# Kernel tuning notes

Hardware: AMD Instinct MI355X
Metric: run time of the kernel (lower is better)

Reference implementation:

```python
import jax, jax.numpy as jnp
import numpy as np

B, S, D, H = 2, 2048, 1024, 16
HD = D // H  # 64


def setup_inputs() -> dict:
    key = jax.random.key(0)
    ks = jax.random.split(key, 10)
    sc = 1.0 / np.sqrt(D)
    return {
        "decoder_hs": jax.random.normal(ks[0], (B, S, D), jnp.float32),
        "encoder_hs": jax.random.normal(ks[1], (B, S, D), jnp.float32),
        "Wq": jax.random.normal(ks[2], (D, D), jnp.float32) * sc,
        "bq": jax.random.normal(ks[3], (D,), jnp.float32) * 0.02,
        "Wk": jax.random.normal(ks[4], (D, D), jnp.float32) * sc,
        "bk": jax.random.normal(ks[5], (D,), jnp.float32) * 0.02,
        "Wv": jax.random.normal(ks[6], (D, D), jnp.float32) * sc,
        "bv": jax.random.normal(ks[7], (D,), jnp.float32) * 0.02,
        "Wp": jax.random.normal(ks[8], (D, D), jnp.float32) * sc,
        "bp": jax.random.normal(ks[9], (D,), jnp.float32) * 0.02,
    }


def reference(decoder_hs, encoder_hs, Wq, bq, Wk, bk, Wv, bv, Wp, bp):
    b, s, d = decoder_hs.shape
    # torch nn.Linear: y = x @ W.T + b, W is [out, in]
    q = decoder_hs @ Wq.T + bq
    k = encoder_hs @ Wk.T + bk
    v = encoder_hs @ Wv.T + bv
    # head split: [b, s, d] -> [b, h, s, hd]
    q = q.reshape(b, s, H, HD).transpose(0, 2, 1, 3)
    k = k.reshape(b, s, H, HD).transpose(0, 2, 1, 3)
    v = v.reshape(b, s, H, HD).transpose(0, 2, 1, 3)
    scale = 1.0 / np.sqrt(HD).astype(np.float32)
    att = jnp.einsum('bhqd,bhkd->bhqk', q, k) * scale
    att = jax.nn.softmax(att, axis=-1)
    y = jnp.einsum('bhqk,bhkd->bhqd', att, v)
    y = y.transpose(0, 2, 1, 3).reshape(b, s, d)
    return y @ Wp.T + bp
```

## Files before the change

kernel.cpp:

```cpp
#include <hip/hip_runtime.h>
#include <hip/hip_bf16.h>
#include <cstdint>
#include <cstddef>

#define BB 2
#define SS 2048
#define DD 1024
#define HH 16
#define HD 64

typedef __attribute__((ext_vector_type(8))) short bf16x8;
typedef __attribute__((ext_vector_type(4))) short bf16x4;
typedef __attribute__((ext_vector_type(4))) float f32x4;

#define MFMA16(va, vb, c) __builtin_amdgcn_mfma_f32_16x16x16bf16_1k(va, vb, c, 0, 0, 0)

#define GLL(g, l) __builtin_amdgcn_global_load_lds( \
    (const __attribute__((address_space(1))) void*)(g), \
    (__attribute__((address_space(3))) void*)(l), 16, 0, 0)

__device__ __forceinline__ short f2bf_fast(float f) {
    uint32_t u = __float_as_uint(f);
    u += 0x7FFF + ((u >> 16) & 1);
    return (short)(u >> 16);
}
__device__ __forceinline__ uint32_t pack_bf2(float a, float b) {
    uint32_t ua = __float_as_uint(a), ub = __float_as_uint(b);
    ua += 0x7FFF + ((ua >> 16) & 1);
    ub += 0x7FFF + ((ub >> 16) & 1);
    return (ua >> 16) | (ub & 0xFFFF0000u);
}
__device__ __forceinline__ bf16x8 cvt8(const float* __restrict__ p) {
    float4 a = *(const float4*)p;
    float4 b = *(const float4*)(p + 4);
    union { uint32_t d[4]; bf16x8 v; } r;
    r.d[0] = pack_bf2(a.x, a.y);
    r.d[1] = pack_bf2(a.z, a.w);
    r.d[2] = pack_bf2(b.x, b.y);
    r.d[3] = pack_bf2(b.z, b.w);
    return r.v;
}

__global__ __launch_bounds__(256) void cvt6_kernel(
    const float* __restrict__ s0, const float* __restrict__ s1,
    const float* __restrict__ s2, const float* __restrict__ s3,
    const float* __restrict__ s4, const float* __restrict__ s5,
    short* __restrict__ d0, short* __restrict__ d1, short* __restrict__ d2,
    short* __restrict__ d3, short* __restrict__ d4, short* __restrict__ d5)
{
    const int z = blockIdx.z;
    const float* s = (z == 0) ? s0 : (z == 1) ? s1 : (z == 2) ? s2
                   : (z == 3) ? s3 : (z == 4) ? s4 : s5;
    short* d = (z == 0) ? d0 : (z == 1) ? d1 : (z == 2) ? d2
             : (z == 3) ? d3 : (z == 4) ? d4 : d5;
    const int n8 = (z < 2) ? (BB * SS * DD / 8) : (DD * DD / 8);
    const int id = blockIdx.x * 256 + threadIdx.x;
    if (id >= n8) return;
    bf16x8 r = cvt8(s + (size_t)id * 8);
    *(uint4*)(d + (size_t)id * 8) = *(uint4*)&r;
}

template<int BF>
__global__ __launch_bounds__(256, 3) void qkv_gemm_kernel(
    const void* __restrict__ dec, const void* __restrict__ enc,
    const void* __restrict__ Wq, const void* __restrict__ Wk,
    const void* __restrict__ Wv,
    const float* __restrict__ bq, const float* __restrict__ bk,
    const float* __restrict__ bv,
    short* __restrict__ Qo, short* __restrict__ Ko, short* __restrict__ Vo)
{
    __shared__ short As[128 * 32];
    __shared__ short Bs[128 * 32];

    const int z = blockIdx.z;
    const void* Xv = (z == 0) ? dec : enc;
    const void* Wp_ = (z == 0) ? Wq : (z == 1) ? Wk : Wv;
    const float* bias = (z == 0) ? bq : (z == 1) ? bk : bv;
    short* Yo = (z == 0) ? Qo : (z == 1) ? Ko : Vo;

    const int t = threadIdx.x;
    const int lane = t & 63, wv = t >> 6;
    const int lr = lane & 15, quad = lane >> 4;
    const int wm = wv >> 1, wn = wv & 1;
    const int m0 = blockIdx.y * 128;
    const int n0 = blockIdx.x * 128;
    const int K = DD;

    f32x4 acc[4][4];
    #pragma unroll
    for (int i = 0; i < 4; i++)
        #pragma unroll
        for (int j = 0; j < 4; j++) acc[i][j] = (f32x4){0.f, 0.f, 0.f, 0.f};

    for (int kb = 0; kb < K; kb += 32) {
        __syncthreads();
        if (BF) {
            const short* Xb = (const short*)Xv;
            const short* Wb = (const short*)Wp_;
            #pragma unroll
            for (int c = 0; c < 2; c++) {
                int r0 = wv * 32 + c * 16;
                int r = r0 + (lane >> 2), ch = (lane & 3) * 8;
                GLL(Xb + (size_t)(m0 + r) * K + kb + ch, &As[r0 * 32]);
                GLL(Wb + (size_t)(n0 + r) * K + kb + ch, &Bs[r0 * 32]);
            }
        } else {
            const float* Xf = (const float*)Xv;
            const float* Wf = (const float*)Wp_;
            #pragma unroll
            for (int c = 0; c < 2; c++) {
                int id = t + c * 256;
                int r = id >> 2, c8 = (id & 3) * 8;
                *(bf16x8*)&As[r * 32 + c8] = cvt8(Xf + (size_t)(m0 + r) * K + kb + c8);
                *(bf16x8*)&Bs[r * 32 + c8] = cvt8(Wf + (size_t)(n0 + r) * K + kb + c8);
            }
        }
        __syncthreads();

        bf16x8 af[4], bfr[4];
        #pragma unroll
        for (int mi = 0; mi < 4; mi++)
            af[mi] = *(const bf16x8*)&As[(wm * 64 + mi * 16 + lr) * 32 + quad * 8];
        #pragma unroll
        for (int ni = 0; ni < 4; ni++)
            bfr[ni] = *(const bf16x8*)&Bs[(wn * 64 + ni * 16 + lr) * 32 + quad * 8];
        #pragma unroll
        for (int mi = 0; mi < 4; mi++)
            #pragma unroll
            for (int ni = 0; ni < 4; ni++)
                acc[mi][ni] = __builtin_amdgcn_mfma_f32_16x16x32_bf16(
                    af[mi], bfr[ni], acc[mi][ni], 0, 0, 0);
    }

    if (z < 2) {
        #pragma unroll
        for (int ni = 0; ni < 4; ni++) {
            int col = n0 + wn * 64 + ni * 16 + lr;
            int h = col >> 6, hd = col & 63;
            float bvv = bias[col];
            #pragma unroll
            for (int mi = 0; mi < 4; mi++) {
                #pragma unroll
                for (int r2 = 0; r2 < 4; r2++) {
                    int row = m0 + wm * 64 + mi * 16 + quad * 4 + r2;
                    int b = row >> 11, s = row & 2047;
                    float v = acc[mi][ni][r2] + bvv;
                    size_t off = ((size_t)(b * HH + h) * SS + s) * HD + hd;
                    Yo[off] = f2bf_fast(v);
                }
            }
        }
    } else {
        #pragma unroll
        for (int ni = 0; ni < 4; ni++) {
            int col = n0 + wn * 64 + ni * 16 + lr;
            int h = col >> 6, hd = col & 63;
            float bvv = bias[col];
            #pragma unroll
            for (int mi = 0; mi < 4; mi++) {
                int s0 = m0 + wm * 64 + mi * 16 + quad * 4;
                int b = s0 >> 11, s = s0 & 2047;
                union { uint32_t d[2]; } u;
                u.d[0] = pack_bf2(acc[mi][ni][0] + bvv, acc[mi][ni][1] + bvv);
                u.d[1] = pack_bf2(acc[mi][ni][2] + bvv, acc[mi][ni][3] + bvv);
                size_t off = ((size_t)(b * HH + h) * HD + hd) * SS + s;
                *(uint2*)(Yo + off) = *(uint2*)&u;
            }
        }
    }
}

template<int WBF>
__global__ __launch_bounds__(256, 2) void proj_gemm_kernel(
    const short* __restrict__ X,
    const void* __restrict__ W, const float* __restrict__ bias,
    float* __restrict__ Y)
{
    __shared__ short As[64 * 32];
    __shared__ short Bs[128 * 32];

    const int t = threadIdx.x;
    const int lane = t & 63, wv = t >> 6;
    const int lr = lane & 15, quad = lane >> 4;
    const int wm = wv >> 1, wn = wv & 1;
    const int m0 = blockIdx.y * 64;
    const int n0 = blockIdx.x * 128;
    const int K = DD, N = DD;

    f32x4 acc[2][4];
    #pragma unroll
    for (int i = 0; i < 2; i++)
        #pragma unroll
        for (int j = 0; j < 4; j++) acc[i][j] = (f32x4){0.f, 0.f, 0.f, 0.f};

    for (int kb = 0; kb < K; kb += 32) {
        __syncthreads();
        {
            int r0 = wv * 16;
            int r = r0 + (lane >> 2), ch = (lane & 3) * 8;
            GLL(X + (size_t)(m0 + r) * K + kb + ch, &As[r0 * 32]);
        }
        if (WBF) {
            const short* Wb = (const short*)W;
            #pragma unroll
            for (int c = 0; c < 2; c++) {
                int r0 = wv * 32 + c * 16;
                int r = r0 + (lane >> 2), ch = (lane & 3) * 8;
                GLL(Wb + (size_t)(n0 + r) * K + kb + ch, &Bs[r0 * 32]);
            }
        } else {
            const float* Wf = (const float*)W;
            #pragma unroll
            for (int c = 0; c < 2; c++) {
                int id = t + c * 256;
                int r = id >> 2, c8 = (id & 3) * 8;
                *(bf16x8*)&Bs[r * 32 + c8] = cvt8(Wf + (size_t)(n0 + r) * K + kb + c8);
            }
        }
        __syncthreads();

        bf16x8 af[2], bfr[4];
        #pragma unroll
        for (int mi = 0; mi < 2; mi++)
            af[mi] = *(const bf16x8*)&As[(wm * 32 + mi * 16 + lr) * 32 + quad * 8];
        #pragma unroll
        for (int ni = 0; ni < 4; ni++)
            bfr[ni] = *(const bf16x8*)&Bs[(wn * 64 + ni * 16 + lr) * 32 + quad * 8];
        #pragma unroll
        for (int mi = 0; mi < 2; mi++)
            #pragma unroll
            for (int ni = 0; ni < 4; ni++)
                acc[mi][ni] = __builtin_amdgcn_mfma_f32_16x16x32_bf16(
                    af[mi], bfr[ni], acc[mi][ni], 0, 0, 0);
    }

    #pragma unroll
    for (int ni = 0; ni < 4; ni++) {
        int col = n0 + wn * 64 + ni * 16 + lr;
        float bvv = bias[col];
        #pragma unroll
        for (int mi = 0; mi < 2; mi++) {
            #pragma unroll
            for (int r2 = 0; r2 < 4; r2++) {
                int row = m0 + wm * 32 + mi * 16 + quad * 4 + r2;
                Y[(size_t)row * N + col] = acc[mi][ni][r2] + bvv;
            }
        }
    }
}

__global__ __launch_bounds__(256, 2) void attn_kernel(
    const short* __restrict__ Q,
    const short* __restrict__ Kgl,
    const short* __restrict__ Vt_g,
    short* __restrict__ Y)
{
    __shared__ short Ks[128][72];
    __shared__ short Vt[64][136];

    const int t = threadIdx.x;
    const int lane = t & 63, w = t >> 6;
    const int lr = lane & 15, quad = lane >> 4;

    const int qt = blockIdx.x & 15;
    const int bh = blockIdx.x >> 4;
    const int b = bh >> 4, h = bh & 15;

    const float C = 0.125f * 1.44269504088896f;

    const short* QpA = Q + ((size_t)bh * SS + qt * 128 + w * 32 + lr) * HD;
    const short* QpB = QpA + 16 * HD;
    bf16x8 qfA0 = *(const bf16x8*)(QpA + quad * 8);
    bf16x8 qfA1 = *(const bf16x8*)(QpA + 32 + quad * 8);
    bf16x8 qfB0 = *(const bf16x8*)(QpB + quad * 8);
    bf16x8 qfB1 = *(const bf16x8*)(QpB + 32 + quad * 8);

    f32x4 oA[4], oB[4];
    #pragma unroll
    for (int i = 0; i < 4; i++) {
        oA[i] = (f32x4){0.f, 0.f, 0.f, 0.f};
        oB[i] = (f32x4){0.f, 0.f, 0.f, 0.f};
    }
    float lsumA = 0.f, lsumB = 0.f;

    const uint4* Kg0 = (const uint4*)(Kgl + (size_t)bh * SS * HD);
    const short* Vg0 = Vt_g + (size_t)bh * HD * SS;

    for (int kt = 0; kt < SS / 128; kt++) {
        __syncthreads();
        const uint4* Kg = Kg0 + (size_t)kt * 128 * 8;
        #pragma unroll
        for (int c = 0; c < 4; c++) {
            int id = t + c * 256;
            int row = id >> 3, h8 = id & 7;
            *(uint4*)&Ks[row][h8 * 8] = Kg[id];
        }
        #pragma unroll
        for (int c = 0; c < 4; c++) {
            int id = t + c * 256;
            int hd = id >> 4, s16 = id & 15;
            *(uint4*)&Vt[hd][s16 * 8] =
                *(const uint4*)(Vg0 + (size_t)hd * SS + kt * 128 + s16 * 8);
        }
        __syncthreads();

        f32x4 scA[8], scB[8];
        #pragma unroll
        for (int nt = 0; nt < 8; nt++) {
            bf16x8 kf0 = *(const bf16x8*)&Ks[nt * 16 + lr][quad * 8];
            bf16x8 kf1 = *(const bf16x8*)&Ks[nt * 16 + lr][32 + quad * 8];
            scA[nt] = __builtin_amdgcn_mfma_f32_16x16x32_bf16(
                kf0, qfA0, (f32x4){0.f, 0.f, 0.f, 0.f}, 0, 0, 0);
            scA[nt] = __builtin_amdgcn_mfma_f32_16x16x32_bf16(kf1, qfA1, scA[nt], 0, 0, 0);
            scB[nt] = __builtin_amdgcn_mfma_f32_16x16x32_bf16(
                kf0, qfB0, (f32x4){0.f, 0.f, 0.f, 0.f}, 0, 0, 0);
            scB[nt] = __builtin_amdgcn_mfma_f32_16x16x32_bf16(kf1, qfB1, scB[nt], 0, 0, 0);
        }

        bf16x4 pbA[8], pbB[8];
        #pragma unroll
        for (int nt = 0; nt < 8; nt++) {
            float a0 = __builtin_amdgcn_exp2f(scA[nt][0] * C);
            float a1 = __builtin_amdgcn_exp2f(scA[nt][1] * C);
            float a2 = __builtin_amdgcn_exp2f(scA[nt][2] * C);
            float a3 = __builtin_amdgcn_exp2f(scA[nt][3] * C);
            lsumA += (a0 + a1) + (a2 + a3);
            union { uint32_t d[2]; bf16x4 v; } ua;
            ua.d[0] = pack_bf2(a0, a1);
            ua.d[1] = pack_bf2(a2, a3);
            pbA[nt] = ua.v;
            float b0 = __builtin_amdgcn_exp2f(scB[nt][0] * C);
            float b1 = __builtin_amdgcn_exp2f(scB[nt][1] * C);
            float b2 = __builtin_amdgcn_exp2f(scB[nt][2] * C);
            float b3 = __builtin_amdgcn_exp2f(scB[nt][3] * C);
            lsumB += (b0 + b1) + (b2 + b3);
            union { uint32_t d[2]; bf16x4 v; } ub;
            ub.d[0] = pack_bf2(b0, b1);
            ub.d[1] = pack_bf2(b2, b3);
            pbB[nt] = ub.v;
        }

        #pragma unroll
        for (int dt = 0; dt < 4; dt++) {
            #pragma unroll
            for (int nt = 0; nt < 8; nt++) {
                bf16x4 va = *(const bf16x4*)&Vt[dt * 16 + lr][nt * 16 + quad * 4];
                oA[dt] = MFMA16(va, pbA[nt], oA[dt]);
                oB[dt] = MFMA16(va, pbB[nt], oB[dt]);
            }
        }
    }

    lsumA += __shfl_xor(lsumA, 16, 64);
    lsumA += __shfl_xor(lsumA, 32, 64);
    lsumB += __shfl_xor(lsumB, 16, 64);
    lsumB += __shfl_xor(lsumB, 32, 64);
    float invA = 1.0f / lsumA, invB = 1.0f / lsumB;

    const int srowA = qt * 128 + w * 32 + lr;
    short* YpA = Y + ((size_t)b * SS + srowA) * DD + h * 64 + quad * 4;
    short* YpB = YpA + 16 * DD;
    #pragma unroll
    for (int dt = 0; dt < 4; dt++) {
        union { uint32_t d[2]; } ua;
        ua.d[0] = pack_bf2(oA[dt][0] * invA, oA[dt][1] * invA);
        ua.d[1] = pack_bf2(oA[dt][2] * invA, oA[dt][3] * invA);
        *(uint2*)(YpA + dt * 16) = *(uint2*)&ua;
        union { uint32_t d[2]; } ub;
        ub.d[0] = pack_bf2(oB[dt][0] * invB, oB[dt][1] * invB);
        ub.d[1] = pack_bf2(oB[dt][2] * invB, oB[dt][3] * invB);
        *(uint2*)(YpB + dt * 16) = *(uint2*)&ub;
    }
}

extern "C" void kernel_launch(void* const* d_in, const int* in_sizes, int n_in,
                              void* d_out, int out_size, void* d_ws, size_t ws_size,
                              hipStream_t stream) {
    const float* dec = (const float*)d_in[0];
    const float* enc = (const float*)d_in[1];
    const float* Wq  = (const float*)d_in[2];
    const float* bq  = (const float*)d_in[3];
    const float* Wk  = (const float*)d_in[4];
    const float* bk  = (const float*)d_in[5];
    const float* Wv  = (const float*)d_in[6];
    const float* bv  = (const float*)d_in[7];
    const float* Wp  = (const float*)d_in[8];
    const float* bp  = (const float*)d_in[9];

    const size_t per = (size_t)BB * HH * SS * HD;
    const size_t wsz = (size_t)DD * DD;
    short* ws = (short*)d_ws;
    short* Qb  = ws;
    short* Kb  = ws + per;
    short* Vtb = ws + 2 * per;
    short* Yb  = ws + 3 * per;

    dim3 qkv_grid(DD / 128, (BB * SS) / 128, 3);
    dim3 proj_grid(DD / 128, (BB * SS) / 64);
    const int attn_blocks = BB * HH * (SS / 128);

    const size_t need = (6 * per + 4 * wsz) * sizeof(short);
    if (ws_size >= need) {
        short* decb = ws + 4 * per;
        short* encb = ws + 5 * per;
        short* Wqb  = ws + 6 * per;
        short* Wkb  = Wqb + wsz;
        short* Wvb  = Wqb + 2 * wsz;
        short* Wpb  = Wqb + 3 * wsz;
        cvt6_kernel<<<dim3((BB * SS * DD / 8 + 255) / 256, 1, 6), 256, 0, stream>>>(
            dec, enc, Wq, Wk, Wv, Wp, decb, encb, Wqb, Wkb, Wvb, Wpb);
        qkv_gemm_kernel<1><<<qkv_grid, 256, 0, stream>>>(
            decb, encb, Wqb, Wkb, Wvb, bq, bk, bv, Qb, Kb, Vtb);
        attn_kernel<<<attn_blocks, 256, 0, stream>>>(Qb, Kb, Vtb, Yb);
        proj_gemm_kernel<1><<<proj_grid, 256, 0, stream>>>(Yb, Wpb, bp, (float*)d_out);
    } else {
        qkv_gemm_kernel<0><<<qkv_grid, 256, 0, stream>>>(
            dec, enc, Wq, Wk, Wv, bq, bk, bv, Qb, Kb, Vtb);
        attn_kernel<<<attn_blocks, 256, 0, stream>>>(Qb, Kb, Vtb, Yb);
        proj_gemm_kernel<0><<<proj_grid, 256, 0, stream>>>(Yb, Wp, bp, (float*)d_out);
    }
}
```

Measured before the change: 215.3 us.

## Prefetch K/V tiles into registers and add mid-workspace bf16 weight path

The attention kernel now loads the next K and V tiles into registers while computing on the current tile, so global load latency overlaps with the MFMA work. The workspace layout is reduced: bf16 activation copies now reuse the Y slot, which lowers the full-path requirement. A new intermediate path converts only the weights to bf16 when the workspace cannot hold activation copies, with the GEMM templated separately on activation and weight precision. The prefetch costs extra registers per thread and may reduce occupancy in the attention kernel.

```diff
diff --git a/kernel.cpp b/kernel.cpp
--- a/kernel.cpp
+++ b/kernel.cpp
@@ -60,7 +60,21 @@
     *(uint4*)(d + (size_t)id * 8) = *(uint4*)&r;
 }
 
-template<int BF>
+__global__ __launch_bounds__(256) void cvtW_kernel(
+    const float* __restrict__ s0, const float* __restrict__ s1,
+    const float* __restrict__ s2, const float* __restrict__ s3,
+    short* __restrict__ d0, short* __restrict__ d1,
+    short* __restrict__ d2, short* __restrict__ d3)
+{
+    const int z = blockIdx.z;
+    const float* s = (z == 0) ? s0 : (z == 1) ? s1 : (z == 2) ? s2 : s3;
+    short* d = (z == 0) ? d0 : (z == 1) ? d1 : (z == 2) ? d2 : d3;
+    const int id = blockIdx.x * 256 + threadIdx.x;
+    bf16x8 r = cvt8(s + (size_t)id * 8);
+    *(uint4*)(d + (size_t)id * 8) = *(uint4*)&r;
+}
+
+template<int XBF, int WBF>
 __global__ __launch_bounds__(256, 3) void qkv_gemm_kernel(
     const void* __restrict__ dec, const void* __restrict__ enc,
     const void* __restrict__ Wq, const void* __restrict__ Wk,
@@ -94,24 +108,37 @@
 
     for (int kb = 0; kb < K; kb += 32) {
         __syncthreads();
-        if (BF) {
+        if (XBF) {
             const short* Xb = (const short*)Xv;
-            const short* Wb = (const short*)Wp_;
             #pragma unroll
             for (int c = 0; c < 2; c++) {
                 int r0 = wv * 32 + c * 16;
                 int r = r0 + (lane >> 2), ch = (lane & 3) * 8;
                 GLL(Xb + (size_t)(m0 + r) * K + kb + ch, &As[r0 * 32]);
-                GLL(Wb + (size_t)(n0 + r) * K + kb + ch, &Bs[r0 * 32]);
             }
         } else {
             const float* Xf = (const float*)Xv;
-            const float* Wf = (const float*)Wp_;
             #pragma unroll
             for (int c = 0; c < 2; c++) {
                 int id = t + c * 256;
                 int r = id >> 2, c8 = (id & 3) * 8;
                 *(bf16x8*)&As[r * 32 + c8] = cvt8(Xf + (size_t)(m0 + r) * K + kb + c8);
+            }
+        }
+        if (WBF) {
+            const short* Wb = (const short*)Wp_;
+            #pragma unroll
+            for (int c = 0; c < 2; c++) {
+                int r0 = wv * 32 + c * 16;
+                int r = r0 + (lane >> 2), ch = (lane & 3) * 8;
+                GLL(Wb + (size_t)(n0 + r) * K + kb + ch, &Bs[r0 * 32]);
+            }
+        } else {
+            const float* Wf = (const float*)Wp_;
+            #pragma unroll
+            for (int c = 0; c < 2; c++) {
+                int id = t + c * 256;
+                int r = id >> 2, c8 = (id & 3) * 8;
                 *(bf16x8*)&Bs[r * 32 + c8] = cvt8(Wf + (size_t)(n0 + r) * K + kb + c8);
             }
         }
@@ -286,21 +313,42 @@
     const uint4* Kg0 = (const uint4*)(Kgl + (size_t)bh * SS * HD);
     const short* Vg0 = Vt_g + (size_t)bh * HD * SS;
 
-    for (int kt = 0; kt < SS / 128; kt++) {
-        __syncthreads();
-        const uint4* Kg = Kg0 + (size_t)kt * 128 * 8;
-        #pragma unroll
-        for (int c = 0; c < 4; c++) {
-            int id = t + c * 256;
-            int row = id >> 3, h8 = id & 7;
-            *(uint4*)&Ks[row][h8 * 8] = Kg[id];
-        }
+    uint4 kreg[4], vreg[4];
+    {
+        const uint4* Kg = Kg0;
+        #pragma unroll
+        for (int c = 0; c < 4; c++) kreg[c] = Kg[t + c * 256];
         #pragma unroll
         for (int c = 0; c < 4; c++) {
             int id = t + c * 256;
             int hd = id >> 4, s16 = id & 15;
-            *(uint4*)&Vt[hd][s16 * 8] =
-                *(const uint4*)(Vg0 + (size_t)hd * SS + kt * 128 + s16 * 8);
+            vreg[c] = *(const uint4*)(Vg0 + (size_t)hd * SS + s16 * 8);
+        }
+    }
+
+    for (int kt = 0; kt < SS / 128; kt++) {
+        __syncthreads();
+        #pragma unroll
+        for (int c = 0; c < 4; c++) {
+            int id = t + c * 256;
+            *(uint4*)&Ks[id >> 3][(id & 7) * 8] = kreg[c];
+        }
+        #pragma unroll
+        for (int c = 0; c < 4; c++) {
+            int id = t + c * 256;
+            int hd = id >> 4, s16 = id & 15;
+            *(uint4*)&Vt[hd][s16 * 8] = vreg[c];
+        }
+        if (kt + 1 < SS / 128) {
+            const uint4* Kg = Kg0 + (size_t)(kt + 1) * 1024;
+            #pragma unroll
+            for (int c = 0; c < 4; c++) kreg[c] = Kg[t + c * 256];
+            #pragma unroll
+            for (int c = 0; c < 4; c++) {
+                int id = t + c * 256;
+                int hd = id >> 4, s16 = id & 15;
+                vreg[c] = *(const uint4*)(Vg0 + (size_t)hd * SS + (kt + 1) * 128 + s16 * 8);
+            }
         }
         __syncthreads();
 
@@ -399,22 +447,35 @@
     dim3 proj_grid(DD / 128, (BB * SS) / 64);
     const int attn_blocks = BB * HH * (SS / 128);
 
-    const size_t need = (6 * per + 4 * wsz) * sizeof(short);
-    if (ws_size >= need) {
-        short* decb = ws + 4 * per;
-        short* encb = ws + 5 * per;
-        short* Wqb  = ws + 6 * per;
+    const size_t need_full = (5 * per + 4 * wsz) * sizeof(short);
+    const size_t need_mid  = (4 * per + wsz) * sizeof(short);
+
+    if (ws_size >= need_full) {
+        short* decb = ws + 3 * per;
+        short* encb = ws + 4 * per;
+        short* Wqb  = ws + 5 * per;
         short* Wkb  = Wqb + wsz;
         short* Wvb  = Wqb + 2 * wsz;
         short* Wpb  = Wqb + 3 * wsz;
         cvt6_kernel<<<dim3((BB * SS * DD / 8 + 255) / 256, 1, 6), 256, 0, stream>>>(
             dec, enc, Wq, Wk, Wv, Wp, decb, encb, Wqb, Wkb, Wvb, Wpb);
-        qkv_gemm_kernel<1><<<qkv_grid, 256, 0, stream>>>(
+        qkv_gemm_kernel<1, 1><<<qkv_grid, 256, 0, stream>>>(
             decb, encb, Wqb, Wkb, Wvb, bq, bk, bv, Qb, Kb, Vtb);
         attn_kernel<<<attn_blocks, 256, 0, stream>>>(Qb, Kb, Vtb, Yb);
         proj_gemm_kernel<1><<<proj_grid, 256, 0, stream>>>(Yb, Wpb, bp, (float*)d_out);
+    } else if (ws_size >= need_mid) {
+        short* Wqb = Yb;
+        short* Wkb = Yb + wsz;
+        short* Wvb = Yb + 2 * wsz;
+        short* Wpb = ws + 4 * per;
+        cvtW_kernel<<<dim3(DD * DD / 8 / 256, 1, 4), 256, 0, stream>>>(
+            Wq, Wk, Wv, Wp, Wqb, Wkb, Wvb, Wpb);
+        qkv_gemm_kernel<0, 1><<<qkv_grid, 256, 0, stream>>>(
+            dec, enc, Wqb, Wkb, Wvb, bq, bk, bv, Qb, Kb, Vtb);
+        attn_kernel<<<attn_blocks, 256, 0, stream>>>(Qb, Kb, Vtb, Yb);
+        proj_gemm_kernel<1><<<proj_grid, 256, 0, stream>>>(Yb, Wpb, bp, (float*)d_out);
     } else {
-        qkv_gemm_kernel<0><<<qkv_grid, 256, 0, stream>>>(
+        qkv_gemm_kernel<0, 0><<<qkv_grid, 256, 0, stream>>>(
             dec, enc, Wq, Wk, Wv, bq, bk, bv, Qb, Kb, Vtb);
         attn_kernel<<<attn_blocks, 256, 0, stream>>>(Qb, Kb, Vtb, Yb);
         proj_gemm_kernel<0><<<proj_grid, 256, 0, stream>>>(Yb, Wp, bp, (float*)d_out);
```

Measured after the change: 252.6 us. +17.3%, slower.
